# Kernel tuning notes

Measured on AMD Instinct MI355X. Metric: run time of the kernel, lower is better.

Reference implementation:

```python
import jax, jax.numpy as jnp
import numpy as np

NB = 10          # number_of_basis (hardcoded in module)
MAX_RADIUS = 3.5
DIM_SH = 16      # spherical harmonics l = 0..3 -> (3+1)^2 components


def spherical_harmonics_l3(vec):
    # real spherical harmonics l=0..3 of the normalized vector,
    # 'component' normalization (each component has unit variance on S^2)
    r = jnp.sqrt(jnp.sum(vec * vec, -1, keepdims=True))
    u = vec / jnp.maximum(r, 1e-9)
    x, y, z = u[..., 0], u[..., 1], u[..., 2]
    s3, s5, s15 = jnp.sqrt(3.0), jnp.sqrt(5.0), jnp.sqrt(15.0)
    c358 = jnp.sqrt(35.0 / 8.0); c218 = jnp.sqrt(21.0 / 8.0)
    sh = [jnp.ones_like(x),
          s3 * x, s3 * y, s3 * z,
          s15 * x * y, s15 * y * z, (s5 / 2) * (3 * z * z - 1),
          s15 * x * z, (s15 / 2) * (x * x - y * y),
          c358 * y * (3 * x * x - y * y), jnp.sqrt(105.0) * x * y * z,
          c218 * y * (5 * z * z - 1), (jnp.sqrt(7.0) / 2) * z * (5 * z * z - 3),
          c218 * x * (5 * z * z - 1), (jnp.sqrt(105.0) / 2) * z * (x * x - y * y),
          c358 * x * (x * x - 3 * y * y)]
    return jnp.stack(sh, -1)  # [E, 16]


def soft_one_hot(r):
    # e3nn soft_one_hot_linspace, basis='smooth_finite', cutoff=True
    values = jnp.linspace(0.0, MAX_RADIUS, NB + 2)[1:-1]
    step = MAX_RADIUS / (NB + 1)
    u = (r[:, None] - values) / step
    mask = jnp.abs(u) < 1.0
    us = jnp.where(mask, u, 0.0)
    y = jnp.where(mask, jnp.exp(-1.0 / (1.0 - us * us)), 0.0)
    return 1.14136 * jnp.exp(2.0) * y * jnp.sqrt(float(NB))  # * number_of_basis**0.5


def soft_unit_step(t):
    ts = jnp.where(t > 0, t, 1.0)
    return jnp.where(t > 0, jnp.exp(-1.0 / ts), 0.0)


def fcnet(e, W1, W2):
    # e3nn FullyConnectedNet([10, 16, weight_numel], act=silu): bias-free,
    # fan-in normalized linear layers
    h = jax.nn.silu(e @ W1 / jnp.sqrt(float(e.shape[-1])))
    return h @ W2 / jnp.sqrt(float(W1.shape[-1]))


def setup_inputs() -> dict:
    key = jax.random.key(0)
    ks = jax.random.split(key, 9)
    N, E, C, DK = 20000, 50000, 16, 8
    pos = jax.random.uniform(ks[0], (N, 3), jnp.float32) * 2.0  # box so most edges < max_radius
    x = jax.random.normal(ks[1], (N, C), jnp.float32)
    Wq = jax.random.normal(ks[2], (C, DK), jnp.float32)
    Wk1 = jax.random.normal(ks[3], (NB, 16), jnp.float32)
    Wk2 = jax.random.normal(ks[4], (16, C * DIM_SH * DK), jnp.float32)
    Wv1 = jax.random.normal(ks[5], (NB, 16), jnp.float32)
    Wv2 = jax.random.normal(ks[6], (16, C * DIM_SH * DK), jnp.float32)
    edge_src = jax.random.randint(ks[7], (E,), 0, N, jnp.int32)
    edge_dst = jax.random.randint(ks[8], (E,), 0, N, jnp.int32)
    return {"pos": pos, "x": x, "Wq": Wq, "Wk1": Wk1, "Wk2": Wk2,
            "Wv1": Wv1, "Wv2": Wv2, "edge_src": edge_src, "edge_dst": edge_dst}


def reference(pos, x, Wq, Wk1, Wk2, Wv1, Wv2, edge_src, edge_dst):
    N, C = x.shape
    E = edge_src.shape[0]
    DK = Wq.shape[1]
    edge_vec = pos[edge_src] - pos[edge_dst]                    # [E, 3]
    r = jnp.sqrt(jnp.sum(edge_vec * edge_vec, -1) + 1e-18)      # [E]
    emb = soft_one_hot(r)                                       # [E, 10]
    cutoff = soft_unit_step(10.0 * (1.0 - r / MAX_RADIUS))      # [E]
    sh = spherical_harmonics_l3(edge_vec)                       # [E, 16]
    # per-edge weight-conditioned tensor products (shared_weights=False)
    wk = fcnet(emb, Wk1, Wk2).reshape(E, C, DIM_SH, DK)
    wv = fcnet(emb, Wv1, Wv2).reshape(E, C, DIM_SH, DK)
    xs = x[edge_src]                                            # gather [E, C]
    norm = jnp.sqrt(float(C * DIM_SH))
    k = jnp.einsum('ec,ej,ecjo->eo', xs, sh, wk) / norm         # [E, DK]
    v = jnp.einsum('ec,ej,ecjo->eo', xs, sh, wv) / norm         # [E, DK]
    q = x @ Wq                                                  # [N, DK]
    logits = jnp.sum(q[edge_dst] * k, -1) / jnp.sqrt(float(DK)) # [E]
    expv = cutoff * jnp.exp(logits)
    z = jax.ops.segment_sum(expv, edge_dst, num_segments=N)     # segment-softmax denom
    z = jnp.where(z == 0.0, 1.0, z)
    alpha = expv / z[edge_dst]
    w = jnp.sqrt(jax.nn.relu(alpha))
    out = jax.ops.segment_sum(w[:, None] * v, edge_dst, num_segments=N)  # [N, DK]
    return out
```

## Files before the change

kernel.cpp:

```cpp
#include <hip/hip_runtime.h>
#include <hip/hip_bf16.h>

#define NBASIS 10
#define CDIM 16
#define DKDIM 8
#define JDIM 16

typedef _Float16 half8 __attribute__((ext_vector_type(8)));
typedef float floatx4 __attribute__((ext_vector_type(4)));

__device__ __forceinline__ float ldf(const void* p, int i, int f32) {
    if (f32) return ((const float*)p)[i];
    return __bfloat162float(((const __hip_bfloat16*)p)[i]);
}

__device__ __forceinline__ int detect_f32(const void* x) {
    unsigned short b = ((const unsigned short*)x)[threadIdx.x & 63];
    float v = __uint_as_float(((unsigned int)b) << 16);
    bool bad = !(fabsf(v) < 1000.0f) || (v != 0.0f && fabsf(v) < 1e-15f);
    unsigned long long m = __ballot(bad);
    return (__popcll(m) >= 8) ? 1 : 0;
}

__device__ __forceinline__ const float* uniform_ptr(const float* p) {
    uint64_t v = (uint64_t)p;
    uint32_t lo = __builtin_amdgcn_readfirstlane((uint32_t)v);
    uint32_t hi = __builtin_amdgcn_readfirstlane((uint32_t)(v >> 32));
    return (const float*)(((uint64_t)hi << 32) | lo);
}

__global__ __launch_bounds__(256) void prep_kernel(
    const void* __restrict__ x, const void* __restrict__ Wq,
    const void* __restrict__ Wk1, const void* __restrict__ Wk2,
    const void* __restrict__ Wv1, const void* __restrict__ Wv2,
    float* __restrict__ w1k, float* __restrict__ w1v,
    float* __restrict__ qbuf, float* __restrict__ zbuf,
    float* __restrict__ outacc, _Float16* __restrict__ Bpk, int N)
{
    const int f32 = detect_f32(x);
    int i = blockIdx.x * 256 + threadIdx.x;
    if (i < 160) { w1k[i] = ldf(Wk1, i, f32); w1v[i] = ldf(Wv1, i, f32); }
    if (i < 65536) {
        int j = i & 7, lane = (i >> 3) & 63, ks = (i >> 9) & 7, nt = i >> 12;
        int kk = ks * 32 + (lane >> 4) * 8 + j;
        int nn = nt * 16 + (lane & 15);
        int c = kk >> 4, jj = kk & 15;
        int net = nn >> 7, m = (nn >> 3) & 15, o = nn & 7;
        float v = ldf(net ? Wv2 : Wk2, m * 2048 + c * 128 + jj * 8 + o, f32);
        Bpk[i] = (_Float16)v;
    }
    if (i < N) zbuf[i] = 0.0f;
    if (i < N * 8) {
        outacc[i] = 0.0f;
        int n = i >> 3, o = i & 7;
        float acc = 0.0f;
        #pragma unroll
        for (int c = 0; c < CDIM; ++c)
            acc = fmaf(ldf(x, n * CDIM + c, f32), ldf(Wq, c * DKDIM + o, f32), acc);
        qbuf[i] = acc;
    }
}

__global__ __launch_bounds__(256) void edge_kernel(
    const void* __restrict__ pos, const void* __restrict__ x,
    const int* __restrict__ esrc, const int* __restrict__ edst,
    const float* __restrict__ w1k, const float* __restrict__ w1v,
    const float* __restrict__ qbuf, const _Float16* __restrict__ Bpk,
    float* __restrict__ zbuf, float* __restrict__ outacc, int E)
{
    __shared__ union {
        struct { float xs[64][17]; float sh[64][17]; } g;
        _Float16 A[16384];
        struct { float pk[2][64][9]; float pv[2][64][9]; } p;
    } u;
    __shared__ _Float16 hm_lds[64][34];
    __shared__ float cut_lds[64];
    __shared__ float evs_lds[64];
    __shared__ int   d_lds[64];

    const int f32  = detect_f32(x);
    const int tid  = threadIdx.x;
    const int lane = tid & 63;
    const int w    = tid >> 6;
    const int q    = lane >> 4;
    const int e0   = blockIdx.x * 64;
    const int e_g  = e0 + lane;
    const int eidx = (e_g < E) ? e_g : (E - 1);
    const int s = esrc[eidx], d = edst[eidx];

    float vx = ldf(pos, s * 3 + 0, f32) - ldf(pos, d * 3 + 0, f32);
    float vy = ldf(pos, s * 3 + 1, f32) - ldf(pos, d * 3 + 1, f32);
    float vz = ldf(pos, s * 3 + 2, f32) - ldf(pos, d * 3 + 2, f32);
    float r2 = vx * vx + vy * vy + vz * vz;
    float r  = sqrtf(r2 + 1e-18f);

    if (w == 0) {
        float rsh = sqrtf(r2);
        float inv = 1.0f / fmaxf(rsh, 1e-9f);
        float ux = vx * inv, uy = vy * inv, uz = vz * inv;
        const float s3   = 1.7320508075688772f;
        const float s5   = 2.23606797749979f;
        const float s15  = 3.872983346207417f;
        const float c358 = 2.091650066335189f;
        const float c218 = 1.6201851746019651f;
        const float s105 = 10.246950765959598f;
        const float s7h  = 1.3228756555322954f;
        float xx = ux * ux, yy = uy * uy, zz = uz * uz;
        float sh[16];
        sh[0] = 1.0f;
        sh[1] = s3 * ux; sh[2] = s3 * uy; sh[3] = s3 * uz;
        sh[4] = s15 * ux * uy;
        sh[5] = s15 * uy * uz;
        sh[6] = 0.5f * s5 * (3.0f * zz - 1.0f);
        sh[7] = s15 * ux * uz;
        sh[8] = 0.5f * s15 * (xx - yy);
        sh[9] = c358 * uy * (3.0f * xx - yy);
        sh[10] = s105 * ux * uy * uz;
        sh[11] = c218 * uy * (5.0f * zz - 1.0f);
        sh[12] = s7h * uz * (5.0f * zz - 3.0f);
        sh[13] = c218 * ux * (5.0f * zz - 1.0f);
        sh[14] = 0.5f * s105 * uz * (xx - yy);
        sh[15] = c358 * ux * (xx - 3.0f * yy);
        #pragma unroll
        for (int j = 0; j < 16; ++j) u.g.sh[lane][j] = sh[j];
        float tcut = 10.0f * (1.0f - r * (1.0f / 3.5f));
        cut_lds[lane] = (tcut > 0.0f) ? expf(-1.0f / tcut) : 0.0f;
        d_lds[lane] = d;
    } else if (w == 1) {
        #pragma unroll
        for (int c = 0; c < CDIM; ++c)
            u.g.xs[lane][c] = ldf(x, s * CDIM + c, f32);
    } else {
        const float* w1 = uniform_ptr((w == 2) ? w1k : w1v);
        const int off = (w == 2) ? 0 : 16;
        float emb[NBASIS];
        const float step = 3.5f / 11.0f;
        const float istep = 11.0f / 3.5f;
        const float coef = (float)(1.14136 * 7.38905609893065 * 3.1622776601683795);
        #pragma unroll
        for (int i = 0; i < NBASIS; ++i) {
            float uu = (r - step * (float)(i + 1)) * istep; uu *= uu;
            emb[i] = (uu < 1.0f) ? coef * expf(-1.0f / (1.0f - uu)) : 0.0f;
        }
        const float inv_s10 = 0.31622776601683794f;
        #pragma unroll
        for (int m = 0; m < 16; ++m) {
            float pre = 0.0f;
            #pragma unroll
            for (int nb = 0; nb < NBASIS; ++nb)
                pre = fmaf(emb[nb], w1[nb * 16 + m], pre);
            pre *= inv_s10;
            hm_lds[lane][off + m] = (_Float16)(pre / (1.0f + expf(-pre)));
        }
    }
    __syncthreads();

    half8 af[8];
    {
        const int erow = w * 16 + (lane & 15);
        const int coff = q >> 1, jj0 = (q & 1) * 8;
        #pragma unroll
        for (int ks = 0; ks < 8; ++ks) {
            float xsv = u.g.xs[erow][ks * 2 + coff];
            half8 a;
            #pragma unroll
            for (int j = 0; j < 8; ++j)
                a[j] = (_Float16)(xsv * u.g.sh[erow][jj0 + j]);
            af[ks] = a;
        }
    }
    __syncthreads();
    {
        half8* Af = (half8*)u.A;
        #pragma unroll
        for (int ks = 0; ks < 8; ++ks)
            Af[(w * 8 + ks) * 64 + lane] = af[ks];
    }
    __syncthreads();

    float part[16];
    #pragma unroll
    for (int i = 0; i < 16; ++i) part[i] = 0.0f;
    const int b3   = (lane >> 3) & 1;
    const int moff = (w >> 1) * 16;
    const half8* Af = (const half8*)u.A;
    const half8* Bf = (const half8*)Bpk;

    #pragma unroll
    for (int rp = 0; rp < 2; ++rp) {
        half8 a0[8], a1[8];
        #pragma unroll
        for (int ks = 0; ks < 8; ++ks) {
            a0[ks] = Af[((2 * rp)     * 8 + ks) * 64 + lane];
            a1[ks] = Af[((2 * rp + 1) * 8 + ks) * 64 + lane];
        }
        floatx4 acc0[4], acc1[4];
        #pragma unroll
        for (int l = 0; l < 4; ++l) {
            acc0[l] = (floatx4){0.f, 0.f, 0.f, 0.f};
            acc1[l] = (floatx4){0.f, 0.f, 0.f, 0.f};
        }
        #pragma unroll
        for (int l = 0; l < 4; ++l) {
            const int nt = 4 * w + l;
            #pragma unroll
            for (int ks = 0; ks < 8; ++ks) {
                half8 b = Bf[(nt * 8 + ks) * 64 + lane];
                acc0[l] = __builtin_amdgcn_mfma_f32_16x16x32_f16(a0[ks], b, acc0[l], 0, 0, 0);
                acc1[l] = __builtin_amdgcn_mfma_f32_16x16x32_f16(a1[ks], b, acc1[l], 0, 0, 0);
            }
        }
        #pragma unroll
        for (int l = 0; l < 4; ++l) {
            const int m = ((4 * w + l) * 2 + b3) & 15;
            #pragma unroll
            for (int rr = 0; rr < 4; ++rr) {
                const int er = q * 4 + rr;
                part[(2 * rp) * 4 + rr] +=
                    (float)hm_lds[(2 * rp) * 16 + er][moff + m] * acc0[l][rr];
                part[(2 * rp + 1) * 4 + rr] +=
                    (float)hm_lds[(2 * rp + 1) * 16 + er][moff + m] * acc1[l][rr];
            }
        }
    }
    #pragma unroll
    for (int i = 0; i < 16; ++i) part[i] += __shfl_xor(part[i], 8, 64);

    __syncthreads();
    if (b3 == 0) {
        const int o = lane & 7;
        #pragma unroll
        for (int i = 0; i < 16; ++i) {
            const int e = (i >> 2) * 16 + q * 4 + (i & 3);
            if (w < 2) u.p.pk[w][e][o] = part[i];
            else       u.p.pv[w - 2][e][o] = part[i];
        }
    }
    __syncthreads();

    if (tid < 64) {
        const int dd = d_lds[tid];
        float logit = 0.0f;
        #pragma unroll
        for (int o = 0; o < 8; ++o) {
            float kv = u.p.pk[0][tid][o] + u.p.pk[1][tid][o];
            logit = fmaf(qbuf[(size_t)dd * 8 + o], kv, logit);
        }
        logit *= (1.0f / 64.0f) * 0.35355339059327373f;
        float ev = cut_lds[tid] * expf(logit);
        if (e0 + tid < E) atomicAdd(&zbuf[dd], ev);
        evs_lds[tid] = sqrtf(ev);
    }
    __syncthreads();

    {
        const int el = tid & 63, op = tid >> 6;
        if (e0 + el < E) {
            const int dd = d_lds[el];
            const float wq = evs_lds[el] * (1.0f / 64.0f);
            float v0 = u.p.pv[0][el][2 * op]     + u.p.pv[1][el][2 * op];
            float v1 = u.p.pv[0][el][2 * op + 1] + u.p.pv[1][el][2 * op + 1];
            atomicAdd(&outacc[(size_t)dd * 8 + 2 * op],     wq * v0);
            atomicAdd(&outacc[(size_t)dd * 8 + 2 * op + 1], wq * v1);
        }
    }
}

__global__ __launch_bounds__(256) void finalize_kernel(
    const float* __restrict__ outacc, const float* __restrict__ zbuf,
    void* __restrict__ out, const void* __restrict__ x, int n)
{
    const int f32 = detect_f32(x);
    int i = blockIdx.x * 256 + threadIdx.x;
    if (i < n) {
        float z = zbuf[i >> 3];
        z = (z == 0.0f) ? 1.0f : z;
        float val = outacc[i] / sqrtf(z);
        if (f32) ((float*)out)[i] = val;
        else ((__hip_bfloat16*)out)[i] = __float2bfloat16(val);
    }
}

extern "C" void kernel_launch(void* const* d_in, const int* in_sizes, int n_in,
                              void* d_out, int out_size, void* d_ws, size_t ws_size,
                              hipStream_t stream)
{
    const void* pos = d_in[0];
    const void* x   = d_in[1];
    const void* Wq  = d_in[2];
    const void* Wk1 = d_in[3];
    const void* Wk2 = d_in[4];
    const void* Wv1 = d_in[5];
    const void* Wv2 = d_in[6];
    const int* esrc = (const int*)d_in[7];
    const int* edst = (const int*)d_in[8];
    const int N = in_sizes[1] / CDIM;
    const int E = in_sizes[7];

    float* ws = (float*)d_ws;
    float* w1k    = ws;
    float* w1v    = w1k + 160;
    float* qbuf   = w1v + 160;
    float* zbuf   = qbuf + (size_t)N * 8;
    float* outacc = zbuf + N;
    _Float16* Bpk = (_Float16*)(outacc + (size_t)N * 8);

    int prep_threads = N * 8 > 65536 ? N * 8 : 65536;
    int prep_blocks = (prep_threads + 255) / 256;
    prep_kernel<<<prep_blocks, 256, 0, stream>>>(x, Wq, Wk1, Wk2, Wv1, Wv2,
                                                 w1k, w1v, qbuf, zbuf, outacc,
                                                 Bpk, N);

    int edge_blocks = (E + 63) / 64;
    edge_kernel<<<edge_blocks, 256, 0, stream>>>(pos, x, esrc, edst,
                                                 w1k, w1v, qbuf, Bpk,
                                                 zbuf, outacc, E);

    finalize_kernel<<<(N * 8 + 255) / 256, 256, 0, stream>>>(
        outacc, zbuf, d_out, x, N * 8);
}
```

Baseline: 113.6 us.

## Restructure MFMA loop over column tiles and transpose hidden-activation LDS layout

The MFMA loop now iterates over column tiles outermost, keeping four row-tile accumulators and loading each B fragment once while re-reading A fragments from LDS per k-step. The previous version held all A fragments in registers. Hidden activations are stored transposed as [net][m][edge], so each lane reads four consecutive edges with one half4 LDS load instead of scattered scalar loads. The q-projection in the prep kernel now uses one thread per node, loading the x row once instead of once per output. The aim is lower register pressure and fewer LDS loads, in exchange for more LDS traffic for A.

```diff
diff --git a/kernel.cpp b/kernel.cpp
--- a/kernel.cpp
+++ b/kernel.cpp
@@ -7,6 +7,7 @@
 #define JDIM 16
 
 typedef _Float16 half8 __attribute__((ext_vector_type(8)));
+typedef _Float16 half4 __attribute__((ext_vector_type(4)));
 typedef float floatx4 __attribute__((ext_vector_type(4)));
 
 __device__ __forceinline__ float ldf(const void* p, int i, int f32) {
@@ -49,16 +50,21 @@
         float v = ldf(net ? Wv2 : Wk2, m * 2048 + c * 128 + jj * 8 + o, f32);
         Bpk[i] = (_Float16)v;
     }
-    if (i < N) zbuf[i] = 0.0f;
-    if (i < N * 8) {
-        outacc[i] = 0.0f;
-        int n = i >> 3, o = i & 7;
-        float acc = 0.0f;
-        #pragma unroll
-        for (int c = 0; c < CDIM; ++c)
-            acc = fmaf(ldf(x, n * CDIM + c, f32), ldf(Wq, c * DKDIM + o, f32), acc);
-        qbuf[i] = acc;
-    }
+    if (i < N) {
+        zbuf[i] = 0.0f;
+        float xr[CDIM];
+        #pragma unroll
+        for (int c = 0; c < CDIM; ++c) xr[c] = ldf(x, i * CDIM + c, f32);
+        #pragma unroll
+        for (int o = 0; o < DKDIM; ++o) {
+            float acc = 0.0f;
+            #pragma unroll
+            for (int c = 0; c < CDIM; ++c)
+                acc = fmaf(xr[c], ldf(Wq, c * DKDIM + o, f32), acc);
+            qbuf[i * DKDIM + o] = acc;
+        }
+    }
+    if (i < N * 8) outacc[i] = 0.0f;
 }
 
 __global__ __launch_bounds__(256) void edge_kernel(
@@ -73,7 +79,7 @@
         _Float16 A[16384];
         struct { float pk[2][64][9]; float pv[2][64][9]; } p;
     } u;
-    __shared__ _Float16 hm_lds[64][34];
+    __shared__ _Float16 hm16[2][16][64];
     __shared__ float cut_lds[64];
     __shared__ float evs_lds[64];
     __shared__ int   d_lds[64];
@@ -132,7 +138,7 @@
             u.g.xs[lane][c] = ldf(x, s * CDIM + c, f32);
     } else {
         const float* w1 = uniform_ptr((w == 2) ? w1k : w1v);
-        const int off = (w == 2) ? 0 : 16;
+        const int net = w - 2;
         float emb[NBASIS];
         const float step = 3.5f / 11.0f;
         const float istep = 11.0f / 3.5f;
@@ -150,7 +156,7 @@
             for (int nb = 0; nb < NBASIS; ++nb)
                 pre = fmaf(emb[nb], w1[nb * 16 + m], pre);
             pre *= inv_s10;
-            hm_lds[lane][off + m] = (_Float16)(pre / (1.0f + expf(-pre)));
+            hm16[net][m][lane] = (_Float16)(pre / (1.0f + expf(-pre)));
         }
     }
     __syncthreads();
@@ -181,46 +187,33 @@
     float part[16];
     #pragma unroll
     for (int i = 0; i < 16; ++i) part[i] = 0.0f;
-    const int b3   = (lane >> 3) & 1;
-    const int moff = (w >> 1) * 16;
+    const int b3  = (lane >> 3) & 1;
+    const int net = w >> 1;
     const half8* Af = (const half8*)u.A;
     const half8* Bf = (const half8*)Bpk;
 
     #pragma unroll
-    for (int rp = 0; rp < 2; ++rp) {
-        half8 a0[8], a1[8];
+    for (int l = 0; l < 4; ++l) {
+        const int nt = 4 * w + l;
+        floatx4 acc[4];
+        #pragma unroll
+        for (int rt = 0; rt < 4; ++rt) acc[rt] = (floatx4){0.f, 0.f, 0.f, 0.f};
         #pragma unroll
         for (int ks = 0; ks < 8; ++ks) {
-            a0[ks] = Af[((2 * rp)     * 8 + ks) * 64 + lane];
-            a1[ks] = Af[((2 * rp + 1) * 8 + ks) * 64 + lane];
-        }
-        floatx4 acc0[4], acc1[4];
-        #pragma unroll
-        for (int l = 0; l < 4; ++l) {
-            acc0[l] = (floatx4){0.f, 0.f, 0.f, 0.f};
-            acc1[l] = (floatx4){0.f, 0.f, 0.f, 0.f};
-        }
-        #pragma unroll
-        for (int l = 0; l < 4; ++l) {
-            const int nt = 4 * w + l;
-            #pragma unroll
-            for (int ks = 0; ks < 8; ++ks) {
-                half8 b = Bf[(nt * 8 + ks) * 64 + lane];
-                acc0[l] = __builtin_amdgcn_mfma_f32_16x16x32_f16(a0[ks], b, acc0[l], 0, 0, 0);
-                acc1[l] = __builtin_amdgcn_mfma_f32_16x16x32_f16(a1[ks], b, acc1[l], 0, 0, 0);
+            half8 b = Bf[(nt * 8 + ks) * 64 + lane];
+            #pragma unroll
+            for (int rt = 0; rt < 4; ++rt) {
+                half8 a = Af[(rt * 8 + ks) * 64 + lane];
+                acc[rt] = __builtin_amdgcn_mfma_f32_16x16x32_f16(a, b, acc[rt], 0, 0, 0);
             }
         }
-        #pragma unroll
-        for (int l = 0; l < 4; ++l) {
-            const int m = ((4 * w + l) * 2 + b3) & 15;
-            #pragma unroll
-            for (int rr = 0; rr < 4; ++rr) {
-                const int er = q * 4 + rr;
-                part[(2 * rp) * 4 + rr] +=
-                    (float)hm_lds[(2 * rp) * 16 + er][moff + m] * acc0[l][rr];
-                part[(2 * rp + 1) * 4 + rr] +=
-                    (float)hm_lds[(2 * rp + 1) * 16 + er][moff + m] * acc1[l][rr];
-            }
+        const int m = (2 * nt + b3) & 15;
+        #pragma unroll
+        for (int rt = 0; rt < 4; ++rt) {
+            half4 hv = *(const half4*)&hm16[net][m][rt * 16 + q * 4];
+            #pragma unroll
+            for (int rr = 0; rr < 4; ++rr)
+                part[rt * 4 + rr] = fmaf((float)hv[rr], acc[rt][rr], part[rt * 4 + rr]);
         }
     }
     #pragma unroll
```

Result: slower. 119.6 us (+5.3%).
